# Optimization experiments

Measured on AMD Instinct MI355X. Metric: run time of the kernel, lower is better.

The kernel has to match this reference:

```python
import jax, jax.numpy as jnp
import numpy as np

N_NODES = 100000
N_EDGES = 1600000
NUM_GRAPHS = 128


def setup_inputs() -> dict:
    key = jax.random.key(0)
    k1, k2, k3, k4, k5, k6 = jax.random.split(key, 6)
    x = jax.random.normal(k1, (N_NODES, 69), dtype=jnp.float32)
    src = jax.random.randint(k2, (N_EDGES,), 0, N_NODES)
    dst = jax.random.randint(k3, (N_EDGES,), 0, N_NODES)
    graph_ids = jnp.sort(jax.random.randint(k4, (N_NODES,), 0, NUM_GRAPHS))
    # Glorot-uniform weights like dgl GraphConv (bias=False)
    lim1 = np.sqrt(6.0 / (69 + 128))
    lim2 = np.sqrt(6.0 / (128 + 64))
    W1 = jax.random.uniform(k5, (69, 128), minval=-lim1, maxval=lim1, dtype=jnp.float32)
    W2 = jax.random.uniform(k6, (128, 64), minval=-lim2, maxval=lim2, dtype=jnp.float32)
    return {"x": x, "W1": W1, "W2": W2, "src": src, "dst": dst, "graph_ids": graph_ids}


def _graph_conv(feat, W, src, dst, inv_sqrt_out, inv_sqrt_in, n_nodes):
    # dgl GraphConv norm='both': D_out^{-1/2} -> SpMM(A) -> D_in^{-1/2} -> W
    h = feat * inv_sqrt_out[:, None]
    agg = jax.ops.segment_sum(h[src], dst, num_segments=n_nodes)  # [N, d]
    agg = agg * inv_sqrt_in[:, None]
    return agg @ W


def reference(x, W1, W2, src, dst, graph_ids):
    n = x.shape[0]
    ones = jnp.ones((src.shape[0],), dtype=x.dtype)
    out_deg = jax.ops.segment_sum(ones, src, num_segments=n)
    in_deg = jax.ops.segment_sum(ones, dst, num_segments=n)
    inv_sqrt_out = jax.lax.rsqrt(jnp.clip(out_deg, 1.0, None))
    inv_sqrt_in = jax.lax.rsqrt(jnp.clip(in_deg, 1.0, None))

    h = _graph_conv(x, W1, src, dst, inv_sqrt_out, inv_sqrt_in, n)
    h = jax.nn.relu(h)
    h = _graph_conv(h, W2, src, dst, inv_sqrt_out, inv_sqrt_in, n)
    h = jax.nn.relu(h)
    # dgl.max_nodes: per-graph max readout -> [num_graphs, 64]
    readout = jax.ops.segment_max(h, graph_ids, num_segments=NUM_GRAPHS)
    return readout
```

## Files before the change

kernel.cpp:

```cpp
#include <hip/hip_runtime.h>

#define N_NODES 100000
#define N_EDGES 1600000
#define NUM_GRAPHS 128

#define BSH 7
#define NBUCK 782
#define NBLKP 512
#define EPB (N_EDGES / NBLKP)
#define SOFF (NBUCK * NBLKP)
#define NSCAN (2 * NBUCK * NBLKP)
#define SCAN_BS 1024
#define NBSC ((NSCAN + SCAN_BS - 1) / SCAN_BS)

__device__ __forceinline__ unsigned bf16pair(float a, float b) {
    unsigned ua = __float_as_uint(a), ub = __float_as_uint(b);
    ua = (ua + 0x7FFFu + ((ua >> 16) & 1u)) >> 16;
    ub = (ub + 0x7FFFu + ((ub >> 16) & 1u)) >> 16;
    return ua | (ub << 16);
}
__device__ __forceinline__ float bflo(unsigned u) { return __uint_as_float(u << 16); }
__device__ __forceinline__ float bfhi(unsigned u) { return __uint_as_float(u & 0xFFFF0000u); }

__global__ __launch_bounds__(256) void part_hist(const int* __restrict__ src,
                                                 const int* __restrict__ dst,
                                                 int* __restrict__ cnt) {
    __shared__ int hd[NBUCK], hs[NBUCK];
    for (int i = threadIdx.x; i < NBUCK; i += 256) { hd[i] = 0; hs[i] = 0; }
    __syncthreads();
    int bk = blockIdx.x;
    int e0 = bk * EPB;
    for (int j = threadIdx.x; j < EPB; j += 256) {
        int e = e0 + j;
        atomicAdd(&hd[dst[e] >> BSH], 1);
        atomicAdd(&hs[src[e] >> BSH], 1);
    }
    __syncthreads();
    for (int i = threadIdx.x; i < NBUCK; i += 256) {
        cnt[i * NBLKP + bk] = hd[i];
        cnt[SOFF + i * NBLKP + bk] = hs[i];
    }
}

__global__ __launch_bounds__(256) void scan1(const int* __restrict__ cnt, int* __restrict__ excl,
                                             int* __restrict__ blksum, int n) {
    __shared__ int tmp[256];
    int t = threadIdx.x;
    int idx0 = blockIdx.x * SCAN_BS + t * 4;
    int v[4];
#pragma unroll
    for (int k = 0; k < 4; ++k) { int i = idx0 + k; v[k] = (i < n) ? cnt[i] : 0; }
    int sum = v[0] + v[1] + v[2] + v[3];
    tmp[t] = sum;
    __syncthreads();
    for (int off = 1; off < 256; off <<= 1) {
        int y = (t >= off) ? tmp[t - off] : 0;
        __syncthreads();
        tmp[t] += y;
        __syncthreads();
    }
    int run = (t > 0) ? tmp[t - 1] : 0;
#pragma unroll
    for (int k = 0; k < 4; ++k) { int i = idx0 + k; if (i < n) excl[i] = run; run += v[k]; }
    if (t == 255) blksum[blockIdx.x] = tmp[255];
}

__global__ __launch_bounds__(256) void scan2(int* __restrict__ blksum, int nb) {
    __shared__ int tmp[256];
    int t = threadIdx.x;
    int C = (nb + 255) / 256;
    int base = t * C;
    int s = 0;
    for (int k = 0; k < C; ++k) { int i = base + k; if (i < nb) s += blksum[i]; }
    tmp[t] = s;
    __syncthreads();
    for (int off = 1; off < 256; off <<= 1) {
        int y = (t >= off) ? tmp[t - off] : 0;
        __syncthreads();
        tmp[t] += y;
        __syncthreads();
    }
    int run = (t > 0) ? tmp[t - 1] : 0;
    for (int k = 0; k < C; ++k) {
        int i = base + k;
        if (i < nb) { int v = blksum[i]; blksum[i] = run; run += v; }
    }
}

__global__ void scan3(int* __restrict__ excl, const int* __restrict__ blkoff, int n) {
    int i = blockIdx.x * 256 + threadIdx.x;
    if (i < n) excl[i] += blkoff[i >> 10];
}

__global__ __launch_bounds__(256) void part_scatter(const int* __restrict__ src,
                                                    const int* __restrict__ dst,
                                                    const int* __restrict__ base,
                                                    unsigned* __restrict__ pdst,
                                                    unsigned char* __restrict__ psrc) {
    __shared__ int cd[NBUCK], cs[NBUCK];
    int bk = blockIdx.x;
    for (int i = threadIdx.x; i < NBUCK; i += 256) {
        cd[i] = base[i * NBLKP + bk];
        cs[i] = base[SOFF + i * NBLKP + bk] - N_EDGES;
    }
    __syncthreads();
    int e0 = bk * EPB;
    for (int j = threadIdx.x; j < EPB; j += 256) {
        int e = e0 + j;
        int s = src[e], d = dst[e];
        int pd = atomicAdd(&cd[d >> BSH], 1);
        pdst[pd] = (unsigned)s | ((unsigned)(d & 127) << 17);
        int ps = atomicAdd(&cs[s >> BSH], 1);
        psrc[ps] = (unsigned char)(s & 127);
    }
}

__global__ __launch_bounds__(256) void build_csr(const unsigned* __restrict__ pdst,
                                                 const int* __restrict__ base,
                                                 int* __restrict__ ecol, int* __restrict__ row_start,
                                                 float* __restrict__ isqi, int nN) {
    __shared__ int lh[128];
    __shared__ int lcur[128];
    int bu = blockIdx.x;
    int b0 = base[bu * NBLKP];
    int b1 = (bu == NBUCK - 1) ? N_EDGES : base[(bu + 1) * NBLKP];
    int t = threadIdx.x;
    if (t < 128) lh[t] = 0;
    __syncthreads();
    for (int j = b0 + t; j < b1; j += 256)
        atomicAdd(&lh[pdst[j] >> 17], 1);
    __syncthreads();
    int myc = (t < 128) ? lh[t] : 0;
    for (int off = 1; off < 128; off <<= 1) {
        int v = (t < 128 && t >= off) ? lh[t - off] : 0;
        __syncthreads();
        if (t < 128) lh[t] += v;
        __syncthreads();
    }
    if (t < 128) {
        int excl = lh[t] - myc;
        int node = (bu << BSH) + t;
        if (node < nN) {
            row_start[node] = b0 + excl;
            isqi[node] = rsqrtf(fmaxf((float)myc, 1.0f));
        }
        lcur[t] = b0 + excl;
    }
    __syncthreads();
    for (int j = b0 + t; j < b1; j += 256) {
        unsigned w = pdst[j];
        int off = w >> 17;
        int pos = atomicAdd(&lcur[off], 1);
        ecol[pos] = (int)(w & 0x1FFFFu);
    }
}

__global__ __launch_bounds__(256) void src_deg_prescale(const unsigned char* __restrict__ psrc,
                                                        const int* __restrict__ base,
                                                        const float* __restrict__ x,
                                                        float* __restrict__ isqo,
                                                        unsigned* __restrict__ xsu, int nN) {
    __shared__ int lh[128];
    __shared__ float sc[128];
    int bu = blockIdx.x;
    int b0 = base[SOFF + bu * NBLKP] - N_EDGES;
    int b1 = (bu == NBUCK - 1) ? N_EDGES : base[SOFF + (bu + 1) * NBLKP] - N_EDGES;
    int t = threadIdx.x;
    if (t < 128) lh[t] = 0;
    __syncthreads();
    for (int j = b0 + t; j < b1; j += 256)
        atomicAdd(&lh[psrc[j]], 1);
    __syncthreads();
    if (t < 128) {
        float v = rsqrtf(fmaxf((float)lh[t], 1.0f));
        sc[t] = v;
        int node = (bu << BSH) + t;
        if (node < nN) isqo[node] = v;
    }
    __syncthreads();
    int n0 = bu << BSH;
    int rows = min(128, nN - n0);
    for (int idx = t; idx < rows * 36; idx += 256) {
        int r = idx / 36, c2 = idx - r * 36;
        float s = sc[r];
        int c = 2 * c2;
        float a = (c < 69) ? x[(size_t)(n0 + r) * 69 + c] * s : 0.0f;
        float b = (c + 1 < 69) ? x[(size_t)(n0 + r) * 69 + c + 1] * s : 0.0f;
        xsu[(size_t)(n0 + r) * 36 + c2] = bf16pair(a, b);
    }
}

__global__ void gather1_kernel(const unsigned* __restrict__ feat, const int* __restrict__ ecol,
                               const int* __restrict__ row_start, const float* __restrict__ dscale,
                               float* __restrict__ agg, int nN, int nE) {
    int wave = (int)(((unsigned)blockIdx.x * blockDim.x + threadIdx.x) >> 6);
    int lane = threadIdx.x & 63;
    if (wave >= nN) return;
    int beg = row_start[wave];
    int end = (wave == nN - 1) ? nE : row_start[wave + 1];
    bool act = (lane < 36);
    float ax = 0.0f, ay = 0.0f;
    for (int j0 = beg; j0 < end; j0 += 64) {
        int ne = min(64, end - j0);
        int eidx = (lane < ne) ? ecol[j0 + lane] : 0;
        int k = 0;
        for (; k + 8 <= ne; k += 8) {
            unsigned v[8];
#pragma unroll
            for (int u = 0; u < 8; ++u) {
                int s = __shfl(eidx, k + u);
                v[u] = act ? feat[(size_t)s * 36 + lane] : 0u;
            }
#pragma unroll
            for (int u = 0; u < 8; ++u) { ax += bflo(v[u]); ay += bfhi(v[u]); }
        }
        for (; k + 2 <= ne; k += 2) {
            int s0 = __shfl(eidx, k), s1 = __shfl(eidx, k + 1);
            unsigned v0 = act ? feat[(size_t)s0 * 36 + lane] : 0u;
            unsigned v1 = act ? feat[(size_t)s1 * 36 + lane] : 0u;
            ax += bflo(v0) + bflo(v1); ay += bfhi(v0) + bfhi(v1);
        }
        for (; k < ne; ++k) {
            int s = __shfl(eidx, k);
            unsigned v = act ? feat[(size_t)s * 36 + lane] : 0u;
            ax += bflo(v); ay += bfhi(v);
        }
    }
    if (act) {
        float dsc = dscale[wave];
        ((float2*)(agg + (size_t)wave * 72))[lane] = make_float2(ax * dsc, ay * dsc);
    }
}

__global__ void gather2_kernel(const unsigned* __restrict__ feat, const int* __restrict__ ecol,
                               const int* __restrict__ row_start, const float* __restrict__ dscale,
                               float* __restrict__ agg, int nN, int nE) {
    int wave = (int)(((unsigned)blockIdx.x * blockDim.x + threadIdx.x) >> 6);
    int lane = threadIdx.x & 63;
    if (wave >= nN) return;
    int beg = row_start[wave];
    int end = (wave == nN - 1) ? nE : row_start[wave + 1];
    int half = lane >> 5;
    int c = lane & 31;
    float ax = 0.0f, ay = 0.0f;
    for (int j0 = beg; j0 < end; j0 += 64) {
        int ne = min(64, end - j0);
        int eidx = (lane < ne) ? ecol[j0 + lane] : 0;
        int k = 0;
        for (; k + 16 <= ne; k += 16) {
            unsigned v[8];
#pragma unroll
            for (int u = 0; u < 8; ++u) {
                int s = __shfl(eidx, k + 2 * u + half);
                v[u] = feat[(size_t)s * 32 + c];
            }
#pragma unroll
            for (int u = 0; u < 8; ++u) { ax += bflo(v[u]); ay += bfhi(v[u]); }
        }
        for (; k + 2 <= ne; k += 2) {
            int s = __shfl(eidx, k + half);
            unsigned v = feat[(size_t)s * 32 + c];
            ax += bflo(v); ay += bfhi(v);
        }
        if (k < ne) {
            int s = __shfl(eidx, k);
            if (half == 0) {
                unsigned v = feat[(size_t)s * 32 + c];
                ax += bflo(v); ay += bfhi(v);
            }
        }
    }
    ax += __shfl_xor(ax, 32);
    ay += __shfl_xor(ay, 32);
    if (half == 0) {
        float dsc = dscale[wave];
        ((float2*)(agg + (size_t)wave * 64))[c] = make_float2(ax * dsc, ay * dsc);
    }
}

template<int KP, int K, int NO, bool RELU, bool SCALE, bool BF16OUT>
__global__ __launch_bounds__(256) void node_gemm(const float* __restrict__ in,
                                                 const float* __restrict__ W,
                                                 const float* __restrict__ rowscale,
                                                 void* __restrict__ out, int nN) {
    constexpr int CG = NO / 8;
    constexpr int RT = 256 / CG;
    constexpr int ROWS = RT * 4;
    __shared__ float Wl[KP * NO];
    for (int i = threadIdx.x; i < KP * NO; i += 256)
        Wl[i] = (i < K * NO) ? W[i] : 0.0f;
    __syncthreads();

    int cg = threadIdx.x % CG;
    int rt = threadIdx.x / CG;
    int row0 = blockIdx.x * ROWS + rt * 4;
    int c0 = cg * 8;

    float4 accL[4] = {};
    float4 accH[4] = {};
    int rclamp[4];
#pragma unroll
    for (int r = 0; r < 4; ++r) rclamp[r] = min(row0 + r, nN - 1);

#pragma unroll 2
    for (int k4 = 0; k4 < KP / 4; ++k4) {
        float4 a[4];
#pragma unroll
        for (int r = 0; r < 4; ++r)
            a[r] = *(const float4*)(in + (size_t)rclamp[r] * KP + k4 * 4);
#pragma unroll
        for (int kk = 0; kk < 4; ++kk) {
            int k = k4 * 4 + kk;
            float4 wlo = *(const float4*)&Wl[k * NO + c0];
            float4 whi = *(const float4*)&Wl[k * NO + c0 + 4];
#pragma unroll
            for (int r = 0; r < 4; ++r) {
                float ar = (kk == 0) ? a[r].x : (kk == 1) ? a[r].y : (kk == 2) ? a[r].z : a[r].w;
                accL[r].x += ar * wlo.x; accL[r].y += ar * wlo.y;
                accL[r].z += ar * wlo.z; accL[r].w += ar * wlo.w;
                accH[r].x += ar * whi.x; accH[r].y += ar * whi.y;
                accH[r].z += ar * whi.z; accH[r].w += ar * whi.w;
            }
        }
    }

#pragma unroll
    for (int r = 0; r < 4; ++r) {
        int row = row0 + r;
        if (row < nN) {
            float4 lo = accL[r], hi = accH[r];
            if (SCALE) {
                float sc = rowscale[row];
                lo.x *= sc; lo.y *= sc; lo.z *= sc; lo.w *= sc;
                hi.x *= sc; hi.y *= sc; hi.z *= sc; hi.w *= sc;
            }
            if (RELU) {
                lo.x = fmaxf(lo.x, 0.f); lo.y = fmaxf(lo.y, 0.f);
                lo.z = fmaxf(lo.z, 0.f); lo.w = fmaxf(lo.w, 0.f);
                hi.x = fmaxf(hi.x, 0.f); hi.y = fmaxf(hi.y, 0.f);
                hi.z = fmaxf(hi.z, 0.f); hi.w = fmaxf(hi.w, 0.f);
            }
            if (BF16OUT) {
                unsigned* ob = (unsigned*)out;
                uint4 p;
                p.x = bf16pair(lo.x, lo.y); p.y = bf16pair(lo.z, lo.w);
                p.z = bf16pair(hi.x, hi.y); p.w = bf16pair(hi.z, hi.w);
                *(uint4*)(ob + (size_t)row * (NO / 2) + c0 / 2) = p;
            } else {
                float* of = (float*)out;
                *(float4*)(of + (size_t)row * NO + c0) = lo;
                *(float4*)(of + (size_t)row * NO + c0 + 4) = hi;
            }
        }
    }
}

__global__ void readout_kernel(const float* __restrict__ agg2, const int* __restrict__ gid,
                               unsigned* __restrict__ out, int nN) {
    const int NPW = 8;
    int wave = (int)(((unsigned)blockIdx.x * blockDim.x + threadIdx.x) >> 6);
    int lane = threadIdx.x & 63;
    int n0 = wave * NPW;
    if (n0 >= nN) return;
    int curg = gid[n0];
    float best = 0.0f;
    for (int i = 0; i < NPW; ++i) {
        int n = n0 + i;
        if (n >= nN) break;
        int g = gid[n];
        float v = fmaxf(agg2[(size_t)n * 64 + lane], 0.0f);
        if (g != curg) {
            atomicMax(&out[curg * 64 + lane], __float_as_uint(best));
            curg = g;
            best = v;
        } else {
            best = fmaxf(best, v);
        }
    }
    atomicMax(&out[curg * 64 + lane], __float_as_uint(best));
}

extern "C" void kernel_launch(void* const* d_in, const int* in_sizes, int n_in,
                              void* d_out, int out_size, void* d_ws, size_t ws_size,
                              hipStream_t stream) {
    const float* x   = (const float*)d_in[0];
    const float* W1  = (const float*)d_in[1];
    const float* W2  = (const float*)d_in[2];
    const int*   src = (const int*)d_in[3];
    const int*   dst = (const int*)d_in[4];
    const int*   gid = (const int*)d_in[5];

    char* w = (char*)d_ws;
    float* isqo    = (float*)w;                 w += N_NODES * 4;
    float* isqi    = (float*)w;                 w += N_NODES * 4;
    int* row_start = (int*)w;                   w += N_NODES * 4;
    int* ecol      = (int*)w;                   w += (size_t)N_EDGES * 4;
    int* cnt       = (int*)w;                   w += (size_t)NSCAN * 4;
    int* blksum    = (int*)w;                   w += 2048 * 4;
    float* bufA    = (float*)w;                 w += (size_t)N_NODES * 72 * 4;
    char* bufB     = w;
    unsigned* pdst      = (unsigned*)bufB;
    unsigned* xsu       = (unsigned*)bufB;
    unsigned char* psrc = (unsigned char*)bufB + (size_t)N_NODES * 36 * 4;
    float* h1           = (float*)bufB;
    float* agg2         = (float*)bufB;

    hipMemsetAsync(d_out, 0, (size_t)out_size * sizeof(float), stream);

    part_hist<<<NBLKP, 256, 0, stream>>>(src, dst, cnt);
    scan1<<<NBSC, 256, 0, stream>>>(cnt, cnt, blksum, NSCAN);
    scan2<<<1, 256, 0, stream>>>(blksum, NBSC);
    scan3<<<(NSCAN + 255) / 256, 256, 0, stream>>>(cnt, blksum, NSCAN);
    part_scatter<<<NBLKP, 256, 0, stream>>>(src, dst, cnt, pdst, psrc);
    build_csr<<<NBUCK, 256, 0, stream>>>(pdst, cnt, ecol, row_start, isqi, N_NODES);
    src_deg_prescale<<<NBUCK, 256, 0, stream>>>(psrc, cnt, x, isqo, xsu, N_NODES);

    gather1_kernel<<<(N_NODES * 64 + 255) / 256, 256, 0, stream>>>(
        xsu, ecol, row_start, isqi, bufA, N_NODES, N_EDGES);
    node_gemm<72, 69, 128, true, false, false><<<(N_NODES + 63) / 64, 256, 0, stream>>>(
        bufA, W1, nullptr, h1, N_NODES);

    node_gemm<128, 128, 64, false, true, true><<<(N_NODES + 127) / 128, 256, 0, stream>>>(
        h1, W2, isqo, (void*)bufA, N_NODES);
    gather2_kernel<<<(N_NODES * 64 + 255) / 256, 256, 0, stream>>>(
        (const unsigned*)bufA, ecol, row_start, isqi, agg2, N_NODES, N_EDGES);

    readout_kernel<<<((N_NODES + 7) / 8 * 64 + 255) / 256, 256, 0, stream>>>(
        agg2, gid, (unsigned*)d_out, N_NODES);
}
```

Measured before the change: 296.7 us.

## Coarsen CSR bucket partitioning, fold scan fixup, vectorize histogram and scatter

Buckets grow from 128 to 1024 nodes, so there are fewer buckets and a smaller count/scan array. The scan3 pass is removed, and consumers add block offsets inline when they read counts. part_hist now uses per-wave privatized shared histograms, and both part_hist and part_scatter read edges with int4 loads. psrc widens to 16-bit local indices, and readout processes 32 nodes per wave. The larger buckets give fewer, longer blocks in build_csr and prescale, which may lower parallelism there.

```diff
diff --git a/kernel.cpp b/kernel.cpp
--- a/kernel.cpp
+++ b/kernel.cpp
@@ -4,9 +4,9 @@
 #define N_EDGES 1600000
 #define NUM_GRAPHS 128
 
-#define BSH 7
-#define NBUCK 782
-#define NBLKP 512
+#define BSH 10
+#define NBUCK 98
+#define NBLKP 500
 #define EPB (N_EDGES / NBLKP)
 #define SOFF (NBUCK * NBLKP)
 #define NSCAN (2 * NBUCK * NBLKP)
@@ -25,20 +25,27 @@
 __global__ __launch_bounds__(256) void part_hist(const int* __restrict__ src,
                                                  const int* __restrict__ dst,
                                                  int* __restrict__ cnt) {
-    __shared__ int hd[NBUCK], hs[NBUCK];
-    for (int i = threadIdx.x; i < NBUCK; i += 256) { hd[i] = 0; hs[i] = 0; }
+    __shared__ int hd[4 * NBUCK], hs[4 * NBUCK];
+    int t = threadIdx.x;
+    for (int i = t; i < 4 * NBUCK; i += 256) { hd[i] = 0; hs[i] = 0; }
+    __syncthreads();
+    int wid = t >> 6;
+    int* hdw = hd + wid * NBUCK;
+    int* hsw = hs + wid * NBUCK;
+    int e0 = blockIdx.x * EPB;
+    for (int j = 4 * t; j + 3 < EPB; j += 1024) {
+        int4 s4 = *(const int4*)(src + e0 + j);
+        int4 d4 = *(const int4*)(dst + e0 + j);
+        atomicAdd(&hdw[d4.x >> BSH], 1); atomicAdd(&hdw[d4.y >> BSH], 1);
+        atomicAdd(&hdw[d4.z >> BSH], 1); atomicAdd(&hdw[d4.w >> BSH], 1);
+        atomicAdd(&hsw[s4.x >> BSH], 1); atomicAdd(&hsw[s4.y >> BSH], 1);
+        atomicAdd(&hsw[s4.z >> BSH], 1); atomicAdd(&hsw[s4.w >> BSH], 1);
+    }
     __syncthreads();
     int bk = blockIdx.x;
-    int e0 = bk * EPB;
-    for (int j = threadIdx.x; j < EPB; j += 256) {
-        int e = e0 + j;
-        atomicAdd(&hd[dst[e] >> BSH], 1);
-        atomicAdd(&hs[src[e] >> BSH], 1);
-    }
-    __syncthreads();
-    for (int i = threadIdx.x; i < NBUCK; i += 256) {
-        cnt[i * NBLKP + bk] = hd[i];
-        cnt[SOFF + i * NBLKP + bk] = hs[i];
+    for (int i = t; i < NBUCK; i += 256) {
+        cnt[i * NBLKP + bk] = hd[i] + hd[NBUCK + i] + hd[2 * NBUCK + i] + hd[3 * NBUCK + i];
+        cnt[SOFF + i * NBLKP + bk] = hs[i] + hs[NBUCK + i] + hs[2 * NBUCK + i] + hs[3 * NBUCK + i];
     }
 }
 
@@ -87,99 +94,122 @@
     }
 }
 
-__global__ void scan3(int* __restrict__ excl, const int* __restrict__ blkoff, int n) {
-    int i = blockIdx.x * 256 + threadIdx.x;
-    if (i < n) excl[i] += blkoff[i >> 10];
-}
-
 __global__ __launch_bounds__(256) void part_scatter(const int* __restrict__ src,
                                                     const int* __restrict__ dst,
-                                                    const int* __restrict__ base,
+                                                    const int* __restrict__ cnt,
+                                                    const int* __restrict__ blk,
                                                     unsigned* __restrict__ pdst,
-                                                    unsigned char* __restrict__ psrc) {
+                                                    unsigned short* __restrict__ psrc) {
     __shared__ int cd[NBUCK], cs[NBUCK];
     int bk = blockIdx.x;
-    for (int i = threadIdx.x; i < NBUCK; i += 256) {
-        cd[i] = base[i * NBLKP + bk];
-        cs[i] = base[SOFF + i * NBLKP + bk] - N_EDGES;
+    int t = threadIdx.x;
+    for (int i = t; i < NBUCK; i += 256) {
+        int ii = i * NBLKP + bk;
+        cd[i] = cnt[ii] + blk[ii >> 10];
+        int jj = SOFF + i * NBLKP + bk;
+        cs[i] = cnt[jj] + blk[jj >> 10] - N_EDGES;
     }
     __syncthreads();
     int e0 = bk * EPB;
-    for (int j = threadIdx.x; j < EPB; j += 256) {
-        int e = e0 + j;
-        int s = src[e], d = dst[e];
-        int pd = atomicAdd(&cd[d >> BSH], 1);
-        pdst[pd] = (unsigned)s | ((unsigned)(d & 127) << 17);
-        int ps = atomicAdd(&cs[s >> BSH], 1);
-        psrc[ps] = (unsigned char)(s & 127);
+    for (int j = 4 * t; j + 3 < EPB; j += 1024) {
+        int4 s4 = *(const int4*)(src + e0 + j);
+        int4 d4 = *(const int4*)(dst + e0 + j);
+        int ss[4] = { s4.x, s4.y, s4.z, s4.w };
+        int dd[4] = { d4.x, d4.y, d4.z, d4.w };
+#pragma unroll
+        for (int u = 0; u < 4; ++u) {
+            int s = ss[u], d = dd[u];
+            int pd = atomicAdd(&cd[d >> BSH], 1);
+            pdst[pd] = (unsigned)s | ((unsigned)(d & 1023) << 17);
+            int ps = atomicAdd(&cs[s >> BSH], 1);
+            psrc[ps] = (unsigned short)(s & 1023);
+        }
     }
 }
 
 __global__ __launch_bounds__(256) void build_csr(const unsigned* __restrict__ pdst,
-                                                 const int* __restrict__ base,
+                                                 const int* __restrict__ cnt,
+                                                 const int* __restrict__ blk,
                                                  int* __restrict__ ecol, int* __restrict__ row_start,
                                                  float* __restrict__ isqi, int nN) {
-    __shared__ int lh[128];
-    __shared__ int lcur[128];
+    __shared__ int lh[1024];
+    __shared__ int lcur[1024];
+    __shared__ int tmp[256];
     int bu = blockIdx.x;
-    int b0 = base[bu * NBLKP];
-    int b1 = (bu == NBUCK - 1) ? N_EDGES : base[(bu + 1) * NBLKP];
-    int t = threadIdx.x;
-    if (t < 128) lh[t] = 0;
+    int i0 = bu * NBLKP;
+    int b0 = cnt[i0] + blk[i0 >> 10];
+    int b1;
+    if (bu == NBUCK - 1) b1 = N_EDGES;
+    else { int i1 = (bu + 1) * NBLKP; b1 = cnt[i1] + blk[i1 >> 10]; }
+    int t = threadIdx.x;
+    lh[t] = 0; lh[t + 256] = 0; lh[t + 512] = 0; lh[t + 768] = 0;
     __syncthreads();
     for (int j = b0 + t; j < b1; j += 256)
         atomicAdd(&lh[pdst[j] >> 17], 1);
     __syncthreads();
-    int myc = (t < 128) ? lh[t] : 0;
-    for (int off = 1; off < 128; off <<= 1) {
-        int v = (t < 128 && t >= off) ? lh[t - off] : 0;
-        __syncthreads();
-        if (t < 128) lh[t] += v;
-        __syncthreads();
-    }
-    if (t < 128) {
-        int excl = lh[t] - myc;
-        int node = (bu << BSH) + t;
+    int v0 = lh[4 * t], v1 = lh[4 * t + 1], v2 = lh[4 * t + 2], v3 = lh[4 * t + 3];
+    tmp[t] = v0 + v1 + v2 + v3;
+    __syncthreads();
+    for (int off = 1; off < 256; off <<= 1) {
+        int y = (t >= off) ? tmp[t - off] : 0;
+        __syncthreads();
+        tmp[t] += y;
+        __syncthreads();
+    }
+    int base = (t > 0) ? tmp[t - 1] : 0;
+    int n0 = bu << BSH;
+    int vv[4] = { v0, v1, v2, v3 };
+#pragma unroll
+    for (int k = 0; k < 4; ++k) {
+        int idx = 4 * t + k;
+        int node = n0 + idx;
         if (node < nN) {
-            row_start[node] = b0 + excl;
-            isqi[node] = rsqrtf(fmaxf((float)myc, 1.0f));
-        }
-        lcur[t] = b0 + excl;
+            row_start[node] = b0 + base;
+            isqi[node] = rsqrtf(fmaxf((float)vv[k], 1.0f));
+        }
+        lcur[idx] = b0 + base;
+        base += vv[k];
     }
     __syncthreads();
     for (int j = b0 + t; j < b1; j += 256) {
         unsigned w = pdst[j];
-        int off = w >> 17;
-        int pos = atomicAdd(&lcur[off], 1);
+        int pos = atomicAdd(&lcur[w >> 17], 1);
         ecol[pos] = (int)(w & 0x1FFFFu);
     }
 }
 
-__global__ __launch_bounds__(256) void src_deg_prescale(const unsigned char* __restrict__ psrc,
-                                                        const int* __restrict__ base,
+__global__ __launch_bounds__(256) void src_deg_prescale(const unsigned short* __restrict__ psrc,
+                                                        const int* __restrict__ cnt,
+                                                        const int* __restrict__ blk,
                                                         const float* __restrict__ x,
                                                         float* __restrict__ isqo,
                                                         unsigned* __restrict__ xsu, int nN) {
-    __shared__ int lh[128];
-    __shared__ float sc[128];
+    __shared__ int lh[1024];
+    __shared__ float sc[1024];
     int bu = blockIdx.x;
-    int b0 = base[SOFF + bu * NBLKP] - N_EDGES;
-    int b1 = (bu == NBUCK - 1) ? N_EDGES : base[SOFF + (bu + 1) * NBLKP] - N_EDGES;
-    int t = threadIdx.x;
-    if (t < 128) lh[t] = 0;
+    int i0 = SOFF + bu * NBLKP;
+    int b0 = cnt[i0] + blk[i0 >> 10] - N_EDGES;
+    int b1;
+    if (bu == NBUCK - 1) b1 = N_EDGES;
+    else { int i1 = SOFF + (bu + 1) * NBLKP; b1 = cnt[i1] + blk[i1 >> 10] - N_EDGES; }
+    int t = threadIdx.x;
+    lh[t] = 0; lh[t + 256] = 0; lh[t + 512] = 0; lh[t + 768] = 0;
     __syncthreads();
     for (int j = b0 + t; j < b1; j += 256)
         atomicAdd(&lh[psrc[j]], 1);
     __syncthreads();
-    if (t < 128) {
-        float v = rsqrtf(fmaxf((float)lh[t], 1.0f));
-        sc[t] = v;
-        int node = (bu << BSH) + t;
+    int n0 = bu << BSH;
+#pragma unroll
+    for (int k = 0; k < 4; ++k) {
+        int idx = t + k * 256;
+        float v = rsqrtf(fmaxf((float)lh[idx], 1.0f));
+        sc[idx] = v;
+        int node = n0 + idx;
         if (node < nN) isqo[node] = v;
     }
     __syncthreads();
-    int n0 = bu << BSH;
-    int rows = min(128, nN - n0);
+    int rows = min(1024, nN - n0);
+    if (rows <= 0) return;
     for (int idx = t; idx < rows * 36; idx += 256) {
         int r = idx / 36, c2 = idx - r * 36;
         float s = sc[r];
@@ -357,7 +387,7 @@
 
 __global__ void readout_kernel(const float* __restrict__ agg2, const int* __restrict__ gid,
                                unsigned* __restrict__ out, int nN) {
-    const int NPW = 8;
+    const int NPW = 32;
     int wave = (int)(((unsigned)blockIdx.x * blockDim.x + threadIdx.x) >> 6);
     int lane = threadIdx.x & 63;
     int n0 = wave * NPW;
@@ -396,24 +426,23 @@
     int* row_start = (int*)w;                   w += N_NODES * 4;
     int* ecol      = (int*)w;                   w += (size_t)N_EDGES * 4;
     int* cnt       = (int*)w;                   w += (size_t)NSCAN * 4;
-    int* blksum    = (int*)w;                   w += 2048 * 4;
+    int* blksum    = (int*)w;                   w += 1024 * 4;
     float* bufA    = (float*)w;                 w += (size_t)N_NODES * 72 * 4;
     char* bufB     = w;
-    unsigned* pdst      = (unsigned*)bufB;
-    unsigned* xsu       = (unsigned*)bufB;
-    unsigned char* psrc = (unsigned char*)bufB + (size_t)N_NODES * 36 * 4;
-    float* h1           = (float*)bufB;
-    float* agg2         = (float*)bufB;
+    unsigned* pdst       = (unsigned*)bufB;
+    unsigned* xsu        = (unsigned*)bufB;
+    unsigned short* psrc = (unsigned short*)(bufB + (size_t)N_NODES * 36 * 4);
+    float* h1            = (float*)bufB;
+    float* agg2          = (float*)bufB;
 
     hipMemsetAsync(d_out, 0, (size_t)out_size * sizeof(float), stream);
 
     part_hist<<<NBLKP, 256, 0, stream>>>(src, dst, cnt);
     scan1<<<NBSC, 256, 0, stream>>>(cnt, cnt, blksum, NSCAN);
     scan2<<<1, 256, 0, stream>>>(blksum, NBSC);
-    scan3<<<(NSCAN + 255) / 256, 256, 0, stream>>>(cnt, blksum, NSCAN);
-    part_scatter<<<NBLKP, 256, 0, stream>>>(src, dst, cnt, pdst, psrc);
-    build_csr<<<NBUCK, 256, 0, stream>>>(pdst, cnt, ecol, row_start, isqi, N_NODES);
-    src_deg_prescale<<<NBUCK, 256, 0, stream>>>(psrc, cnt, x, isqo, xsu, N_NODES);
+    part_scatter<<<NBLKP, 256, 0, stream>>>(src, dst, cnt, blksum, pdst, psrc);
+    build_csr<<<NBUCK, 256, 0, stream>>>(pdst, cnt, blksum, ecol, row_start, isqi, N_NODES);
+    src_deg_prescale<<<NBUCK, 256, 0, stream>>>(psrc, cnt, blksum, x, isqo, xsu, N_NODES);
 
     gather1_kernel<<<(N_NODES * 64 + 255) / 256, 256, 0, stream>>>(
         xsu, ecol, row_start, isqi, bufA, N_NODES, N_EDGES);
@@ -425,6 +454,6 @@
     gather2_kernel<<<(N_NODES * 64 + 255) / 256, 256, 0, stream>>>(
         (const unsigned*)bufA, ecol, row_start, isqi, agg2, N_NODES, N_EDGES);
 
-    readout_kernel<<<((N_NODES + 7) / 8 * 64 + 255) / 256, 256, 0, stream>>>(
+    readout_kernel<<<((N_NODES + 31) / 32 * 64 + 255) / 256, 256, 0, stream>>>(
         agg2, gid, (unsigned*)d_out, N_NODES);
 }
```

Result: slower. 363.5 us (+22.5%).
